# Kernel tuning notes

Measured on AMD Instinct MI355X. Metric: run time of the kernel, lower is better.

The kernel has to match this reference:

```python
import jax, jax.numpy as jnp
import numpy as np

H = 8  # head_count


def setup_inputs() -> dict:
    key = jax.random.key(0)
    ks = jax.random.split(key, 9)
    n, C, w = 8, 512, 8192
    Kc, Vc = 512, 512
    s = 0.02
    return {
        "x": jax.random.normal(ks[0], (n, C, w), dtype=jnp.float32),
        "Wk": jax.random.normal(ks[1], (Kc, C), dtype=jnp.float32) * s,
        "bk": jax.random.normal(ks[2], (Kc,), dtype=jnp.float32) * s,
        "Wq": jax.random.normal(ks[3], (Kc, C), dtype=jnp.float32) * s,
        "bq": jax.random.normal(ks[4], (Kc,), dtype=jnp.float32) * s,
        "Wv": jax.random.normal(ks[5], (Vc, C), dtype=jnp.float32) * s,
        "bv": jax.random.normal(ks[6], (Vc,), dtype=jnp.float32) * s,
        "Wr": jax.random.normal(ks[7], (C, Vc), dtype=jnp.float32) * s,
        "br": jax.random.normal(ks[8], (C,), dtype=jnp.float32) * s,
    }


def reference(x, Wk, bk, Wq, bq, Wv, bv, Wr, br):
    n, C, w = x.shape
    Kc, Vc = Wk.shape[0], Wv.shape[0]
    hk, hv = Kc // H, Vc // H
    # 1x1 Conv1d == channel-mixing GEMM
    keys = jnp.einsum('kc,ncw->nkw', Wk, x) + bk[None, :, None]
    queries = jnp.einsum('kc,ncw->nkw', Wq, x) + bq[None, :, None]
    values = jnp.einsum('vc,ncw->nvw', Wv, x) + bv[None, :, None]
    # split heads: [n, H, hd, w]
    K = jax.nn.softmax(keys.reshape(n, H, hk, w), axis=-1)   # softmax over positions
    Q = jax.nn.softmax(queries.reshape(n, H, hk, w), axis=2)  # softmax over channels
    V = values.reshape(n, H, hv, w)
    # context = K @ V^T : [n, H, hk, hv]
    ctx = jnp.einsum('nhkw,nhvw->nhkv', K, V)
    # attended = ctx^T @ Q : [n, H, hv, w]
    att = jnp.einsum('nhkv,nhkw->nhvw', ctx, Q).reshape(n, Vc, w)
    out = jnp.einsum('cv,nvw->ncw', Wr, att) + br[None, :, None] + x
    return out
```

## Files before the change

kernel.cpp:

```cpp
#include <hip/hip_runtime.h>
#include <hip/hip_bf16.h>
#include <cstdint>

#define NB 8
#define CD 512
#define WD 8192
#define NH 8

typedef __bf16 bf16x8 __attribute__((ext_vector_type(8)));
typedef float  f32x4  __attribute__((ext_vector_type(4)));
typedef float  f32x16 __attribute__((ext_vector_type(16)));

__device__ __forceinline__ void gload_lds16(const __bf16* g, __bf16* l) {
  __builtin_amdgcn_global_load_lds((const __attribute__((address_space(1))) void*)g,
                                   (__attribute__((address_space(3))) void*)l,
                                   16, 0, 0);
}

__global__ void __launch_bounds__(256) prep_x_kernel(const float* __restrict__ x,
                                                     __bf16* __restrict__ xT) {
  __shared__ float tile[64][65];
  const int n = blockIdx.z, cb = blockIdx.y * 64, wb = blockIdx.x * 64;
  const int t = threadIdx.x;
  const int t63 = t & 63, tg = t >> 6;
  const float* xp = x + ((size_t)n * CD + cb) * WD + wb;
#pragma unroll
  for (int i = 0; i < 16; i++) {
    const int cc = tg * 16 + i;
    tile[cc][t63] = xp[(size_t)cc * WD + t63];
  }
  __syncthreads();
  __bf16* op = xT + ((size_t)n * WD + wb) * CD + cb;
#pragma unroll
  for (int i = 0; i < 16; i++) {
    const int ww = tg * 16 + i;
    op[(size_t)ww * CD + t63] = (__bf16)tile[t63][ww];
  }
}

__global__ void __launch_bounds__(256) prep_w_kernel(const float* __restrict__ Wk,
                                                     const float* __restrict__ Wq,
                                                     const float* __restrict__ Wv,
                                                     const float* __restrict__ Wr,
                                                     const float* __restrict__ bk,
                                                     const float* __restrict__ bv,
                                                     __bf16* __restrict__ WkvB,
                                                     __bf16* __restrict__ WqB,
                                                     __bf16* __restrict__ WrB,
                                                     float* __restrict__ bkv) {
  const int gid = blockIdx.x * 256 + threadIdx.x;
  WkvB[gid]          = (__bf16)Wk[gid];
  WkvB[262144 + gid] = (__bf16)Wv[gid];
  WqB[gid]           = (__bf16)Wq[gid];
  WrB[gid]           = (__bf16)Wr[gid];
  if (gid < 512)       bkv[gid] = bk[gid];
  else if (gid < 1024) bkv[gid] = bv[gid - 512];
}

#define STAGE_SLAB(Ak, Bk, lds, t)                                          \
  _Pragma("unroll") for (int rnd = 0; rnd < 8; rnd++) {                     \
    const int c = rnd * 256 + (t);                                          \
    const int cc = c & 1023;                                                \
    const int r = cc >> 3;                                                  \
    const int g = (cc & 7) ^ (r & 7);                                       \
    const __bf16* src = ((c >> 10) ? (Bk) : (Ak)) + (size_t)r * 512 + g * 8;\
    gload_lds16(src, (lds) + (size_t)c * 8);                                \
  }

__device__ __forceinline__ void gemm_lds_core(const __bf16* __restrict__ A,
                                              const __bf16* __restrict__ B,
                                              f32x4 (&acc)[4][4], __bf16* lds) {
  const int t = threadIdx.x;
  const int lane = t & 63, wave = t >> 6;
  const int l15 = lane & 15, quad = lane >> 4;
  const int wm = (wave >> 1) << 6, wn = (wave & 1) << 6;
#pragma unroll 1
  for (int kc = 0; kc < 8; kc++) {
    const __bf16* Ak = A + kc * 64;
    const __bf16* Bk = B + kc * 64;
    STAGE_SLAB(Ak, Bk, lds, t)
    __syncthreads();
#pragma unroll
    for (int k0 = 0; k0 < 2; k0++) {
      const int gk = k0 * 4 + quad;
      bf16x8 av[4], bv[4];
#pragma unroll
      for (int i = 0; i < 4; i++) {
        const int r = wm + i * 16 + l15;
        av[i] = *(const bf16x8*)(lds + (size_t)((r << 3) + (gk ^ (r & 7))) * 8);
      }
#pragma unroll
      for (int j = 0; j < 4; j++) {
        const int r = wn + j * 16 + l15;
        bv[j] = *(const bf16x8*)(lds + (size_t)(8192 + (r << 3) + (gk ^ (r & 7))) * 8);
      }
#pragma unroll
      for (int i = 0; i < 4; i++)
#pragma unroll
        for (int j = 0; j < 4; j++)
          acc[i][j] = __builtin_amdgcn_mfma_f32_16x16x32_bf16(av[i], bv[j], acc[i][j], 0, 0, 0);
    }
    __syncthreads();
  }
}

__device__ __forceinline__ void gemm_lds_core32(const __bf16* __restrict__ A,
                                                const __bf16* __restrict__ B,
                                                f32x16 (&acc)[2][2], __bf16* lds) {
  const int t = threadIdx.x;
  const int lane = t & 63, wave = t >> 6;
  const int l31 = lane & 31, khalf = lane >> 5;
  const int wm = (wave >> 1) << 6, wn = (wave & 1) << 6;
#pragma unroll 1
  for (int kc = 0; kc < 8; kc++) {
    const __bf16* Ak = A + kc * 64;
    const __bf16* Bk = B + kc * 64;
    STAGE_SLAB(Ak, Bk, lds, t)
    __syncthreads();
#pragma unroll
    for (int kk = 0; kk < 4; kk++) {
      const int g = kk * 2 + khalf;
      bf16x8 av[2], bv[2];
#pragma unroll
      for (int i = 0; i < 2; i++) {
        const int r = wm + i * 32 + l31;
        av[i] = *(const bf16x8*)(lds + (size_t)((r << 3) + (g ^ (r & 7))) * 8);
      }
#pragma unroll
      for (int j = 0; j < 2; j++) {
        const int r = wn + j * 32 + l31;
        bv[j] = *(const bf16x8*)(lds + (size_t)(8192 + (r << 3) + (g ^ (r & 7))) * 8);
      }
#pragma unroll
      for (int i = 0; i < 2; i++)
#pragma unroll
        for (int j = 0; j < 2; j++)
          acc[i][j] = __builtin_amdgcn_mfma_f32_32x32x16_bf16(av[i], bv[j], acc[i][j], 0, 0, 0);
    }
    __syncthreads();
  }
}

__global__ void __launch_bounds__(256) gemm_kv_kernel(const __bf16* __restrict__ WkvB,
                                                      const __bf16* __restrict__ xT,
                                                      const float* __restrict__ bkv,
                                                      __bf16* __restrict__ kv) {
  __shared__ __bf16 lds[16384];
  const int n = blockIdx.z, m0 = blockIdx.y * 128, w0 = blockIdx.x * 128;
  f32x16 acc[2][2];
#pragma unroll
  for (int i = 0; i < 2; i++)
#pragma unroll
    for (int j = 0; j < 2; j++)
#pragma unroll
      for (int r = 0; r < 16; r++) acc[i][j][r] = 0.f;
  gemm_lds_core32(WkvB + (size_t)m0 * 512, xT + ((size_t)n * WD + w0) * 512, acc, lds);
  const int t = threadIdx.x, lane = t & 63, wave = t >> 6;
  const int l31 = lane & 31, khalf = lane >> 5;
  const int wm = (wave >> 1) << 6, wn = (wave & 1) << 6;
  __bf16* outp = kv + (size_t)n * 1024 * WD + w0 + wn + l31;
#pragma unroll
  for (int i = 0; i < 2; i++)
#pragma unroll
    for (int reg = 0; reg < 16; reg++) {
      const int row = (reg & 3) + 8 * (reg >> 2) + 4 * khalf;
      const int m = m0 + wm + i * 32 + row;
      const float bias = bkv[m];
      __bf16* rp = outp + (size_t)m * WD;
#pragma unroll
      for (int j = 0; j < 2; j++) rp[j * 32] = (__bf16)(acc[i][j][reg] + bias);
    }
}

__global__ void __launch_bounds__(256) gemm_qT_kernel(const __bf16* __restrict__ xT,
                                                      const __bf16* __restrict__ WqB,
                                                      const float* __restrict__ bq,
                                                      __bf16* __restrict__ qT) {
  __shared__ __bf16 lds[16384];
  const int n = blockIdx.z, w0 = blockIdx.x * 128, q0 = blockIdx.y * 128;
  f32x4 acc[4][4];
#pragma unroll
  for (int i = 0; i < 4; i++)
#pragma unroll
    for (int j = 0; j < 4; j++) acc[i][j] = (f32x4){0.f, 0.f, 0.f, 0.f};
  gemm_lds_core(xT + ((size_t)n * WD + w0) * 512, WqB + (size_t)q0 * 512, acc, lds);
  const int t = threadIdx.x, lane = t & 63, wave = t >> 6;
  const int l15 = lane & 15, quad = lane >> 4;
  const int wm = (wave >> 1) << 6, wn = (wave & 1) << 6;
  float bqv[4];
#pragma unroll
  for (int j = 0; j < 4; j++) bqv[j] = bq[q0 + wn + j * 16 + l15];
#pragma unroll
  for (int i = 0; i < 4; i++)
#pragma unroll
    for (int r = 0; r < 4; r++) {
      float e[4];
      float s = 0.f;
#pragma unroll
      for (int j = 0; j < 4; j++) {
        e[j] = __expf(acc[i][j][r] + bqv[j]);
        s += e[j];
      }
      s += __shfl_xor(s, 1);
      s += __shfl_xor(s, 2);
      s += __shfl_xor(s, 4);
      s += __shfl_xor(s, 8);
      const float inv = 1.0f / s;
      const int w = w0 + wm + i * 16 + quad * 4 + r;
      __bf16* rp = qT + ((size_t)n * WD + w) * 512 + q0 + wn + l15;
#pragma unroll
      for (int j = 0; j < 4; j++) rp[j * 16] = (__bf16)(e[j] * inv);
    }
}

__global__ void __launch_bounds__(256) gemm_out_kernel(const __bf16* __restrict__ Mf,
                                                       const __bf16* __restrict__ qT,
                                                       const float* __restrict__ br,
                                                       const float* __restrict__ x,
                                                       float* __restrict__ out) {
  __shared__ __bf16 lds[16384];
  const int n = blockIdx.z, c0 = blockIdx.y * 128, w0 = blockIdx.x * 128;
  f32x16 acc[2][2];
#pragma unroll
  for (int i = 0; i < 2; i++)
#pragma unroll
    for (int j = 0; j < 2; j++)
#pragma unroll
      for (int r = 0; r < 16; r++) acc[i][j][r] = 0.f;
  gemm_lds_core32(Mf + ((size_t)n * 512 + c0) * 512, qT + ((size_t)n * WD + w0) * 512, acc, lds);
  const int t = threadIdx.x, lane = t & 63, wave = t >> 6;
  const int l31 = lane & 31, khalf = lane >> 5;
  const int wm = (wave >> 1) << 6, wn = (wave & 1) << 6;
#pragma unroll
  for (int i = 0; i < 2; i++)
#pragma unroll
    for (int reg = 0; reg < 16; reg++) {
      const int row = (reg & 3) + 8 * (reg >> 2) + 4 * khalf;
      const int c = c0 + wm + i * 32 + row;
      const float bias = br[c];
      const size_t base = ((size_t)n * CD + c) * WD + w0 + wn + l31;
#pragma unroll
      for (int j = 0; j < 2; j++)
        out[base + j * 32] = acc[i][j][reg] + bias + x[base + j * 32];
    }
}

__global__ void __launch_bounds__(256) ctx_kernel(const __bf16* __restrict__ kv,
                                                  float* __restrict__ partial,
                                                  float* __restrict__ ssum) {
  const int chunk = blockIdx.x, h = blockIdx.y, n = blockIdx.z;
  const int t = threadIdx.x, lane = t & 63, wave = t >> 6;
  const int l15 = lane & 15, quad = lane >> 4;
  const int krow = h * 64 + wave * 16 + l15;
  const __bf16* Kp = kv + ((size_t)n * 1024 + krow) * WD + chunk * 1024 + quad * 8;
  const __bf16* Vp = kv + ((size_t)n * 1024 + 512 + h * 64 + l15) * WD + chunk * 1024 + quad * 8;
  f32x4 acc[4];
#pragma unroll
  for (int j = 0; j < 4; j++) acc[j] = (f32x4){0.f, 0.f, 0.f, 0.f};
  float esum = 0.f;
  for (int s = 0; s < 32; s++) {
    bf16x8 kraw = *(const bf16x8*)(Kp + s * 32);
    bf16x8 af;
#pragma unroll
    for (int e = 0; e < 8; e++) {
      const float ev = __expf((float)kraw[e]);
      esum += ev;
      af[e] = (__bf16)ev;
    }
#pragma unroll
    for (int j = 0; j < 4; j++) {
      bf16x8 bv = *(const bf16x8*)(Vp + (size_t)(j * 16) * WD + s * 32);
      acc[j] = __builtin_amdgcn_mfma_f32_16x16x32_bf16(af, bv, acc[j], 0, 0, 0);
    }
  }
  esum += __shfl_xor(esum, 16);
  esum += __shfl_xor(esum, 32);
  float* pp = partial + (((size_t)(n * 8 + h) * 8 + chunk) << 12);
#pragma unroll
  for (int j = 0; j < 4; j++)
#pragma unroll
    for (int r = 0; r < 4; r++) {
      const int kr = wave * 16 + quad * 4 + r;
      const int vc = j * 16 + l15;
      pp[kr * 64 + vc] = acc[j][r];
    }
  if (lane < 16)
    ssum[(((size_t)(n * 8 + h) * 8 + chunk) << 6) + wave * 16 + l15] = esum;
}

__global__ void __launch_bounds__(256) ctx_reduce_kernel(const float* __restrict__ partial,
                                                         const float* __restrict__ ssum,
                                                         __bf16* __restrict__ ctxB) {
  const int gid = blockIdx.x * 256 + threadIdx.x;
  const int nh = gid >> 12;
  const int kvi = gid & 4095;
  const int k = kvi >> 6;
  float s = 0.f;
#pragma unroll
  for (int c = 0; c < 8; c++) s += ssum[(((size_t)nh * 8 + c) << 6) + k];
  const float* pp = partial + ((size_t)nh << 15) + kvi;
  float v = 0.f;
#pragma unroll
  for (int c = 0; c < 8; c++) v += pp[(size_t)c << 12];
  ctxB[gid] = (__bf16)(v / s);
}

__global__ void __launch_bounds__(256) mfuse_kernel(const __bf16* __restrict__ WrB,
                                                    const __bf16* __restrict__ ctxB,
                                                    __bf16* __restrict__ Mf) {
  const int ms = blockIdx.x, h = blockIdx.y, n = blockIdx.z;
  const int t = threadIdx.x, lane = t & 63, wave = t >> 6;
  const int l15 = lane & 15, quad = lane >> 4;
  f32x4 acc[2][4];
#pragma unroll
  for (int i = 0; i < 2; i++)
#pragma unroll
    for (int j = 0; j < 4; j++) acc[i][j] = (f32x4){0.f, 0.f, 0.f, 0.f};
  const __bf16* Ap = WrB + (size_t)(ms * 128 + wave * 32 + l15) * 512 + h * 64 + quad * 8;
  const __bf16* Bp = ctxB + ((size_t)(n * 8 + h) << 12) + (size_t)l15 * 64 + quad * 8;
#pragma unroll
  for (int k0 = 0; k0 < 64; k0 += 32) {
    bf16x8 av[2];
#pragma unroll
    for (int i = 0; i < 2; i++) av[i] = *(const bf16x8*)(Ap + i * 16 * 512 + k0);
#pragma unroll
    for (int j = 0; j < 4; j++) {
      bf16x8 bv = *(const bf16x8*)(Bp + j * 16 * 64 + k0);
#pragma unroll
      for (int i = 0; i < 2; i++)
        acc[i][j] = __builtin_amdgcn_mfma_f32_16x16x32_bf16(av[i], bv, acc[i][j], 0, 0, 0);
    }
  }
#pragma unroll
  for (int i = 0; i < 2; i++)
#pragma unroll
    for (int j = 0; j < 4; j++)
#pragma unroll
      for (int r = 0; r < 4; r++) {
        const int c = ms * 128 + wave * 32 + i * 16 + quad * 4 + r;
        const int col = h * 64 + j * 16 + l15;
        Mf[((size_t)n * 512 + c) * 512 + col] = (__bf16)acc[i][j][r];
      }
}

extern "C" void kernel_launch(void* const* d_in, const int* in_sizes, int n_in,
                              void* d_out, int out_size, void* d_ws, size_t ws_size,
                              hipStream_t stream) {
  (void)in_sizes; (void)n_in; (void)out_size; (void)ws_size;
  const float* x  = (const float*)d_in[0];
  const float* Wk = (const float*)d_in[1];
  const float* bk = (const float*)d_in[2];
  const float* Wq = (const float*)d_in[3];
  const float* bq = (const float*)d_in[4];
  const float* Wv = (const float*)d_in[5];
  const float* bv = (const float*)d_in[6];
  const float* Wr = (const float*)d_in[7];
  const float* br = (const float*)d_in[8];
  float* out = (float*)d_out;

  char* ws = (char*)d_ws;
  __bf16* xT      = (__bf16*)ws;
  float*  partial = (float*)ws;
  __bf16* ctxB    = (__bf16*)(ws + (16ull << 20));
  __bf16* Mf      = (__bf16*)(ws + (20ull << 20));
  __bf16* kv      = (__bf16*)(ws + (64ull << 20));
  __bf16* qT      = (__bf16*)(ws + (192ull << 20));

  char* scr = (char*)d_out + (124ull << 20);
  __bf16* WkvB = (__bf16*)scr;
  __bf16* WqB  = (__bf16*)(scr + (1ull << 20));
  __bf16* WrB  = (__bf16*)(scr + (1536ull << 10));
  float*  bkv  = (float*)(scr + (2ull << 20));
  float*  ssum = (float*)(scr + (2ull << 20) + 65536);

  prep_x_kernel<<<dim3(128, 8, 8), 256, 0, stream>>>(x, xT);
  prep_w_kernel<<<dim3(1024), 256, 0, stream>>>(Wk, Wq, Wv, Wr, bk, bv, WkvB, WqB, WrB, bkv);
  gemm_kv_kernel<<<dim3(64, 8, 8), 256, 0, stream>>>(WkvB, xT, bkv, kv);
  gemm_qT_kernel<<<dim3(64, 4, 8), 256, 0, stream>>>(xT, WqB, bq, qT);
  ctx_kernel<<<dim3(8, 8, 8), 256, 0, stream>>>(kv, partial, ssum);
  ctx_reduce_kernel<<<dim3(1024), 256, 0, stream>>>(partial, ssum, ctxB);
  mfuse_kernel<<<dim3(4, 8, 8), 256, 0, stream>>>(WrB, ctxB, Mf);
  gemm_out_kernel<<<dim3(64, 4, 8), 256, 0, stream>>>(Mf, qT, br, x, out);
}
```

Before: 502.9 us.

## Rewrite KV projection GEMM with 256x256 tiles and double-buffered async LDS pipeline

Measured after the change: 515.3 us. 2.5% more time.

```diff
diff --git a/kernel.cpp b/kernel.cpp
--- a/kernel.cpp
+++ b/kernel.cpp
@@ -141,34 +141,138 @@
   }
 }
 
-__global__ void __launch_bounds__(256) gemm_kv_kernel(const __bf16* __restrict__ WkvB,
-                                                      const __bf16* __restrict__ xT,
-                                                      const float* __restrict__ bkv,
-                                                      __bf16* __restrict__ kv) {
-  __shared__ __bf16 lds[16384];
-  const int n = blockIdx.z, m0 = blockIdx.y * 128, w0 = blockIdx.x * 128;
-  f32x16 acc[2][2];
-#pragma unroll
-  for (int i = 0; i < 2; i++)
-#pragma unroll
-    for (int j = 0; j < 2; j++)
-#pragma unroll
-      for (int r = 0; r < 16; r++) acc[i][j][r] = 0.f;
-  gemm_lds_core32(WkvB + (size_t)m0 * 512, xT + ((size_t)n * WD + w0) * 512, acc, lds);
-  const int t = threadIdx.x, lane = t & 63, wave = t >> 6;
-  const int l31 = lane & 31, khalf = lane >> 5;
-  const int wm = (wave >> 1) << 6, wn = (wave & 1) << 6;
-  __bf16* outp = kv + (size_t)n * 1024 * WD + w0 + wn + l31;
-#pragma unroll
-  for (int i = 0; i < 2; i++)
-#pragma unroll
-    for (int reg = 0; reg < 16; reg++) {
-      const int row = (reg & 3) + 8 * (reg >> 2) + 4 * khalf;
-      const int m = m0 + wm + i * 32 + row;
+__device__ __forceinline__ void stage_chunk(const __bf16* __restrict__ g, __bf16* l, int row0) {
+  const int lane = threadIdx.x & 63;
+  const int r = row0 + (lane >> 3);
+  const int sg = lane & 7;
+  const int gk = sg ^ (r & 7);
+  gload_lds16(g + (size_t)r * 512 + gk * 8, l + (((r << 3) + sg) << 3));
+}
+
+__device__ __forceinline__ void stage_a_unit(const __bf16* __restrict__ g, __bf16* l, int u) {
+  const int w8 = (threadIdx.x >> 6) << 3;
+  stage_chunk(g, l, u * 64 + w8);
+  stage_chunk(g, l, 128 + u * 64 + w8);
+}
+
+__device__ __forceinline__ void stage_b_unit(const __bf16* __restrict__ g, __bf16* l, int v) {
+  const int w = threadIdx.x >> 6;
+  const int r0 = ((w & 3) << 3) + ((w >> 2) << 6) + (v << 5);
+  stage_chunk(g, l, r0);
+  stage_chunk(g, l, 128 + r0);
+}
+
+#define CKPT(N) asm volatile("s_waitcnt vmcnt(" #N ")" ::: "memory")
+
+#define PHASE(BSEL, MH, NH, STAGE_STMT, CKPT_STMT)                              \
+  do {                                                                          \
+    const __bf16* lA = lds + (BSEL) * 32768;                                    \
+    const __bf16* lB = lds + (BSEL) * 32768 + 16384;                            \
+    bf16x8 av[4][2], bv[2][2];                                                  \
+    _Pragma("unroll") for (int ks = 0; ks < 2; ks++) {                          \
+      const int gko = (ks * 4 + quad) ^ (l15 & 7);       \
+      _Pragma("unroll") for (int mi = 0; mi < 4; mi++) {                        \
+        const int r = wm128 + (MH) * 64 + mi * 16 + l15;                        \
+        av[mi][ks] = *(const bf16x8*)(lA + (((r << 3) + gko) << 3));            \
+      }                                                                         \
+      _Pragma("unroll") for (int nj = 0; nj < 2; nj++) {                        \
+        const int r = wn64 + (NH) * 32 + nj * 16 + l15;                         \
+        bv[nj][ks] = *(const bf16x8*)(lB + (((r << 3) + gko) << 3));            \
+      }                                                                         \
+    }                                                                           \
+    STAGE_STMT;                                                                 \
+    __builtin_amdgcn_s_barrier();                                               \
+    asm volatile("s_waitcnt lgkmcnt(0)" ::: "memory");                          \
+    __builtin_amdgcn_sched_barrier(0);                                          \
+    __builtin_amdgcn_s_setprio(1);                                              \
+    _Pragma("unroll") for (int ks = 0; ks < 2; ks++)                            \
+      _Pragma("unroll") for (int mi = 0; mi < 4; mi++)                          \
+        _Pragma("unroll") for (int nj = 0; nj < 2; nj++)                        \
+          acc[(MH) * 4 + mi][(NH) * 2 + nj] =                                   \
+              __builtin_amdgcn_mfma_f32_16x16x32_bf16(                          \
+                  av[mi][ks], bv[nj][ks], acc[(MH) * 4 + mi][(NH) * 2 + nj],    \
+                  0, 0, 0);                                                     \
+    __builtin_amdgcn_s_setprio(0);                                              \
+    CKPT_STMT;                                                                  \
+    __builtin_amdgcn_s_barrier();                                               \
+  } while (0)
+
+__global__ void __launch_bounds__(512, 2) gemm_kv_kernel(const __bf16* __restrict__ WkvB,
+                                                         const __bf16* __restrict__ xT,
+                                                         const float* __restrict__ bkv,
+                                                         __bf16* __restrict__ kv) {
+  extern __shared__ __bf16 lds[];
+  const int t = threadIdx.x;
+  const int lane = t & 63;
+  const int l15 = lane & 15, quad = lane >> 4;
+  const int wave = t >> 6;
+  const int wm128 = (wave >> 2) << 7;
+  const int wn64 = (wave & 3) << 6;
+
+  const int bid = blockIdx.x;
+  const int swz = (bid & 7) * 128 + (bid >> 3);
+  const int m0 = (swz & 3) << 8;
+  const int w0 = ((swz >> 2) & 31) << 8;
+  const int n = swz >> 7;
+
+  const __bf16* Ab = WkvB + (size_t)m0 * 512;
+  const __bf16* Bb = xT + ((size_t)n * WD + w0) * 512;
+
+  f32x4 acc[8][4];
+#pragma unroll
+  for (int i = 0; i < 8; i++)
+#pragma unroll
+    for (int j = 0; j < 4; j++) acc[i][j] = (f32x4){0.f, 0.f, 0.f, 0.f};
+
+  __bf16* const lA0 = lds;
+  __bf16* const lB0 = lds + 16384;
+  __bf16* const lA1 = lds + 32768;
+  __bf16* const lB1 = lds + 49152;
+
+  stage_a_unit(Ab, lA0, 0);
+  stage_b_unit(Bb, lB0, 0);
+  stage_a_unit(Ab, lA0, 1);
+  stage_b_unit(Bb, lB0, 1);
+  stage_a_unit(Ab + 64, lA1, 0);
+  stage_b_unit(Bb + 64, lB1, 0);
+  asm volatile("s_waitcnt vmcnt(4)" ::: "memory");
+  __builtin_amdgcn_s_barrier();
+
+#pragma unroll 1
+  for (int i = 0; i < 3; i++) {
+    const __bf16* As1 = Ab + (2 * i + 1) * 64;
+    const __bf16* Bs1 = Bb + (2 * i + 1) * 64;
+    const __bf16* As2 = Ab + (2 * i + 2) * 64;
+    const __bf16* Bs2 = Bb + (2 * i + 2) * 64;
+    const __bf16* As3 = Ab + (2 * i + 3) * 64;
+    const __bf16* Bs3 = Bb + (2 * i + 3) * 64;
+    PHASE(0, 0, 0, stage_a_unit(As1, lA1, 1), (void)0);
+    PHASE(0, 0, 1, stage_b_unit(Bs1, lB1, 1), (void)0);
+    PHASE(0, 1, 0, stage_a_unit(As2, lA0, 0), (void)0);
+    PHASE(0, 1, 1, stage_b_unit(Bs2, lB0, 0), CKPT(4));
+    PHASE(1, 0, 0, stage_a_unit(As2, lA0, 1), (void)0);
+    PHASE(1, 0, 1, stage_b_unit(Bs2, lB0, 1), (void)0);
+    PHASE(1, 1, 0, stage_a_unit(As3, lA1, 0), (void)0);
+    PHASE(1, 1, 1, stage_b_unit(Bs3, lB1, 0), CKPT(4));
+  }
+  PHASE(0, 0, 0, stage_a_unit(Ab + 7 * 64, lA1, 1), (void)0);
+  PHASE(0, 0, 1, stage_b_unit(Bb + 7 * 64, lB1, 1), (void)0);
+  PHASE(0, 1, 0, (void)0, (void)0);
+  PHASE(0, 1, 1, (void)0, CKPT(0));
+  PHASE(1, 0, 0, (void)0, (void)0);
+  PHASE(1, 0, 1, (void)0, (void)0);
+  PHASE(1, 1, 0, (void)0, (void)0);
+  PHASE(1, 1, 1, (void)0, (void)0);
+
+#pragma unroll
+  for (int MI = 0; MI < 8; MI++)
+#pragma unroll
+    for (int r = 0; r < 4; r++) {
+      const int m = m0 + wm128 + MI * 16 + quad * 4 + r;
       const float bias = bkv[m];
-      __bf16* rp = outp + (size_t)m * WD;
-#pragma unroll
-      for (int j = 0; j < 2; j++) rp[j * 32] = (__bf16)(acc[i][j][reg] + bias);
+      __bf16* rp = kv + ((size_t)n * 1024 + m) * WD + w0 + wn64 + l15;
+#pragma unroll
+      for (int j = 0; j < 4; j++) rp[j * 16] = (__bf16)(acc[MI][j][r] + bias);
     }
 }
 
@@ -375,7 +479,9 @@
 
   prep_x_kernel<<<dim3(128, 8, 8), 256, 0, stream>>>(x, xT);
   prep_w_kernel<<<dim3(1024), 256, 0, stream>>>(Wk, Wq, Wv, Wr, bk, bv, WkvB, WqB, WrB, bkv);
-  gemm_kv_kernel<<<dim3(64, 8, 8), 256, 0, stream>>>(WkvB, xT, bkv, kv);
+  hipFuncSetAttribute((const void*)gemm_kv_kernel,
+                      hipFuncAttributeMaxDynamicSharedMemorySize, 131072);
+  gemm_kv_kernel<<<dim3(1024), dim3(512), 131072, stream>>>(WkvB, xT, bkv, kv);
   gemm_qT_kernel<<<dim3(64, 4, 8), 256, 0, stream>>>(xT, WqB, bq, qT);
   ctx_kernel<<<dim3(8, 8, 8), 256, 0, stream>>>(kv, partial, ssum);
   ctx_reduce_kernel<<<dim3(1024), 256, 0, stream>>>(partial, ssum, ctxB);
```

## Merge KV and Q projection GEMMs, fuse ctx reduce with Mf, widen x transpose

Applied to the files above, without the earlier changes.

New measurement: 504.6 us. About the same (+0.3%).

```diff
diff --git a/kernel.cpp b/kernel.cpp
--- a/kernel.cpp
+++ b/kernel.cpp
@@ -7,6 +7,7 @@
 #define WD 8192
 #define NH 8
 
+typedef __bf16 bf16x2 __attribute__((ext_vector_type(2)));
 typedef __bf16 bf16x8 __attribute__((ext_vector_type(8)));
 typedef float  f32x4  __attribute__((ext_vector_type(4)));
 typedef float  f32x16 __attribute__((ext_vector_type(16)));
@@ -19,14 +20,14 @@
 
 __global__ void __launch_bounds__(256) prep_x_kernel(const float* __restrict__ x,
                                                      __bf16* __restrict__ xT) {
-  __shared__ float tile[64][65];
-  const int n = blockIdx.z, cb = blockIdx.y * 64, wb = blockIdx.x * 64;
+  __shared__ float tile[128][65];
+  const int n = blockIdx.z, cb = blockIdx.y * 128, wb = blockIdx.x * 64;
   const int t = threadIdx.x;
   const int t63 = t & 63, tg = t >> 6;
   const float* xp = x + ((size_t)n * CD + cb) * WD + wb;
 #pragma unroll
-  for (int i = 0; i < 16; i++) {
-    const int cc = tg * 16 + i;
+  for (int i = 0; i < 32; i++) {
+    const int cc = tg * 32 + i;
     tile[cc][t63] = xp[(size_t)cc * WD + t63];
   }
   __syncthreads();
@@ -34,7 +35,9 @@
 #pragma unroll
   for (int i = 0; i < 16; i++) {
     const int ww = tg * 16 + i;
-    op[(size_t)ww * CD + t63] = (__bf16)tile[t63][ww];
+    const float a = tile[t63 * 2][ww];
+    const float b = tile[t63 * 2 + 1][ww];
+    *(bf16x2*)(op + (size_t)ww * CD + t63 * 2) = (bf16x2){(__bf16)a, (__bf16)b};
   }
 }
 
@@ -141,76 +144,76 @@
   }
 }
 
-__global__ void __launch_bounds__(256) gemm_kv_kernel(const __bf16* __restrict__ WkvB,
-                                                      const __bf16* __restrict__ xT,
-                                                      const float* __restrict__ bkv,
-                                                      __bf16* __restrict__ kv) {
+__global__ void __launch_bounds__(256) gemm_kvq_kernel(const __bf16* __restrict__ WkvB,
+                                                       const __bf16* __restrict__ WqB,
+                                                       const __bf16* __restrict__ xT,
+                                                       const float* __restrict__ bkv,
+                                                       const float* __restrict__ bq,
+                                                       __bf16* __restrict__ kv,
+                                                       __bf16* __restrict__ qT) {
   __shared__ __bf16 lds[16384];
-  const int n = blockIdx.z, m0 = blockIdx.y * 128, w0 = blockIdx.x * 128;
-  f32x16 acc[2][2];
-#pragma unroll
-  for (int i = 0; i < 2; i++)
-#pragma unroll
-    for (int j = 0; j < 2; j++)
-#pragma unroll
-      for (int r = 0; r < 16; r++) acc[i][j][r] = 0.f;
-  gemm_lds_core32(WkvB + (size_t)m0 * 512, xT + ((size_t)n * WD + w0) * 512, acc, lds);
+  const int n = blockIdx.z, w0 = blockIdx.x * 128;
   const int t = threadIdx.x, lane = t & 63, wave = t >> 6;
-  const int l31 = lane & 31, khalf = lane >> 5;
-  const int wm = (wave >> 1) << 6, wn = (wave & 1) << 6;
-  __bf16* outp = kv + (size_t)n * 1024 * WD + w0 + wn + l31;
-#pragma unroll
-  for (int i = 0; i < 2; i++)
-#pragma unroll
-    for (int reg = 0; reg < 16; reg++) {
-      const int row = (reg & 3) + 8 * (reg >> 2) + 4 * khalf;
-      const int m = m0 + wm + i * 32 + row;
-      const float bias = bkv[m];
-      __bf16* rp = outp + (size_t)m * WD;
-#pragma unroll
-      for (int j = 0; j < 2; j++) rp[j * 32] = (__bf16)(acc[i][j][reg] + bias);
-    }
-}
-
-__global__ void __launch_bounds__(256) gemm_qT_kernel(const __bf16* __restrict__ xT,
-                                                      const __bf16* __restrict__ WqB,
-                                                      const float* __restrict__ bq,
-                                                      __bf16* __restrict__ qT) {
-  __shared__ __bf16 lds[16384];
-  const int n = blockIdx.z, w0 = blockIdx.x * 128, q0 = blockIdx.y * 128;
-  f32x4 acc[4][4];
-#pragma unroll
-  for (int i = 0; i < 4; i++)
-#pragma unroll
-    for (int j = 0; j < 4; j++) acc[i][j] = (f32x4){0.f, 0.f, 0.f, 0.f};
-  gemm_lds_core(xT + ((size_t)n * WD + w0) * 512, WqB + (size_t)q0 * 512, acc, lds);
-  const int t = threadIdx.x, lane = t & 63, wave = t >> 6;
-  const int l15 = lane & 15, quad = lane >> 4;
-  const int wm = (wave >> 1) << 6, wn = (wave & 1) << 6;
-  float bqv[4];
-#pragma unroll
-  for (int j = 0; j < 4; j++) bqv[j] = bq[q0 + wn + j * 16 + l15];
-#pragma unroll
-  for (int i = 0; i < 4; i++)
-#pragma unroll
-    for (int r = 0; r < 4; r++) {
-      float e[4];
-      float s = 0.f;
-#pragma unroll
-      for (int j = 0; j < 4; j++) {
-        e[j] = __expf(acc[i][j][r] + bqv[j]);
-        s += e[j];
-      }
-      s += __shfl_xor(s, 1);
-      s += __shfl_xor(s, 2);
-      s += __shfl_xor(s, 4);
-      s += __shfl_xor(s, 8);
-      const float inv = 1.0f / s;
-      const int w = w0 + wm + i * 16 + quad * 4 + r;
-      __bf16* rp = qT + ((size_t)n * WD + w) * 512 + q0 + wn + l15;
-#pragma unroll
-      for (int j = 0; j < 4; j++) rp[j * 16] = (__bf16)(e[j] * inv);
-    }
+
+  if (blockIdx.y < 8) {
+    const int m0 = blockIdx.y * 128;
+    f32x16 acc[2][2];
+#pragma unroll
+    for (int i = 0; i < 2; i++)
+#pragma unroll
+      for (int j = 0; j < 2; j++)
+#pragma unroll
+        for (int r = 0; r < 16; r++) acc[i][j][r] = 0.f;
+    gemm_lds_core32(WkvB + (size_t)m0 * 512, xT + ((size_t)n * WD + w0) * 512, acc, lds);
+    const int l31 = lane & 31, khalf = lane >> 5;
+    const int wm = (wave >> 1) << 6, wn = (wave & 1) << 6;
+    __bf16* outp = kv + (size_t)n * 1024 * WD + w0 + wn + l31;
+#pragma unroll
+    for (int i = 0; i < 2; i++)
+#pragma unroll
+      for (int reg = 0; reg < 16; reg++) {
+        const int row = (reg & 3) + 8 * (reg >> 2) + 4 * khalf;
+        const int m = m0 + wm + i * 32 + row;
+        const float bias = bkv[m];
+        __bf16* rp = outp + (size_t)m * WD;
+#pragma unroll
+        for (int j = 0; j < 2; j++) rp[j * 32] = (__bf16)(acc[i][j][reg] + bias);
+      }
+  } else {
+    const int q0 = (blockIdx.y - 8) * 128;
+    f32x4 acc[4][4];
+#pragma unroll
+    for (int i = 0; i < 4; i++)
+#pragma unroll
+      for (int j = 0; j < 4; j++) acc[i][j] = (f32x4){0.f, 0.f, 0.f, 0.f};
+    gemm_lds_core(xT + ((size_t)n * WD + w0) * 512, WqB + (size_t)q0 * 512, acc, lds);
+    const int l15 = lane & 15, quad = lane >> 4;
+    const int wm = (wave >> 1) << 6, wn = (wave & 1) << 6;
+    float bqv[4];
+#pragma unroll
+    for (int j = 0; j < 4; j++) bqv[j] = bq[q0 + wn + j * 16 + l15];
+#pragma unroll
+    for (int i = 0; i < 4; i++)
+#pragma unroll
+      for (int r = 0; r < 4; r++) {
+        float e[4];
+        float s = 0.f;
+#pragma unroll
+        for (int j = 0; j < 4; j++) {
+          e[j] = __expf(acc[i][j][r] + bqv[j]);
+          s += e[j];
+        }
+        s += __shfl_xor(s, 1);
+        s += __shfl_xor(s, 2);
+        s += __shfl_xor(s, 4);
+        s += __shfl_xor(s, 8);
+        const float inv = 1.0f / s;
+        const int w = w0 + wm + i * 16 + quad * 4 + r;
+        __bf16* rp = qT + ((size_t)n * WD + w) * 512 + q0 + wn + l15;
+#pragma unroll
+        for (int j = 0; j < 4; j++) rp[j * 16] = (__bf16)(e[j] * inv);
+      }
+  }
 }
 
 __global__ void __launch_bounds__(256) gemm_out_kernel(const __bf16* __restrict__ Mf,
@@ -288,59 +291,66 @@
     ssum[(((size_t)(n * 8 + h) * 8 + chunk) << 6) + wave * 16 + l15] = esum;
 }
 
-__global__ void __launch_bounds__(256) ctx_reduce_kernel(const float* __restrict__ partial,
+__global__ void __launch_bounds__(256) ctx_finish_kernel(const float* __restrict__ partial,
                                                          const float* __restrict__ ssum,
-                                                         __bf16* __restrict__ ctxB) {
-  const int gid = blockIdx.x * 256 + threadIdx.x;
-  const int nh = gid >> 12;
-  const int kvi = gid & 4095;
-  const int k = kvi >> 6;
-  float s = 0.f;
-#pragma unroll
-  for (int c = 0; c < 8; c++) s += ssum[(((size_t)nh * 8 + c) << 6) + k];
-  const float* pp = partial + ((size_t)nh << 15) + kvi;
-  float v = 0.f;
-#pragma unroll
-  for (int c = 0; c < 8; c++) v += pp[(size_t)c << 12];
-  ctxB[gid] = (__bf16)(v / s);
-}
-
-__global__ void __launch_bounds__(256) mfuse_kernel(const __bf16* __restrict__ WrB,
-                                                    const __bf16* __restrict__ ctxB,
-                                                    __bf16* __restrict__ Mf) {
-  const int ms = blockIdx.x, h = blockIdx.y, n = blockIdx.z;
-  const int t = threadIdx.x, lane = t & 63, wave = t >> 6;
+                                                         const __bf16* __restrict__ WrB,
+                                                         __bf16* __restrict__ Mf) {
+  __shared__ __bf16 ctx_tile[64][72];
+  __shared__ float srow[64];
+  const int h = blockIdx.x, n = blockIdx.y;
+  const int nh = n * 8 + h;
+  const int t = threadIdx.x;
+  if (t < 64) {
+    float s = 0.f;
+#pragma unroll
+    for (int c = 0; c < 8; c++) s += ssum[(((size_t)nh * 8 + c) << 6) + t];
+    srow[t] = 1.0f / s;
+  }
+  __syncthreads();
+  const float* pp = partial + ((size_t)nh << 15);
+#pragma unroll
+  for (int i = 0; i < 16; i++) {
+    const int kvi = i * 256 + t;
+    float v = 0.f;
+#pragma unroll
+    for (int c = 0; c < 8; c++) v += pp[((size_t)c << 12) + kvi];
+    ctx_tile[kvi >> 6][kvi & 63] = (__bf16)(v * srow[kvi >> 6]);
+  }
+  __syncthreads();
+  const int lane = t & 63, wave = t >> 6;
   const int l15 = lane & 15, quad = lane >> 4;
-  f32x4 acc[2][4];
-#pragma unroll
-  for (int i = 0; i < 2; i++)
-#pragma unroll
-    for (int j = 0; j < 4; j++) acc[i][j] = (f32x4){0.f, 0.f, 0.f, 0.f};
-  const __bf16* Ap = WrB + (size_t)(ms * 128 + wave * 32 + l15) * 512 + h * 64 + quad * 8;
-  const __bf16* Bp = ctxB + ((size_t)(n * 8 + h) << 12) + (size_t)l15 * 64 + quad * 8;
-#pragma unroll
-  for (int k0 = 0; k0 < 64; k0 += 32) {
-    bf16x8 av[2];
-#pragma unroll
-    for (int i = 0; i < 2; i++) av[i] = *(const bf16x8*)(Ap + i * 16 * 512 + k0);
-#pragma unroll
-    for (int j = 0; j < 4; j++) {
-      bf16x8 bv = *(const bf16x8*)(Bp + j * 16 * 64 + k0);
-#pragma unroll
-      for (int i = 0; i < 2; i++)
-        acc[i][j] = __builtin_amdgcn_mfma_f32_16x16x32_bf16(av[i], bv, acc[i][j], 0, 0, 0);
-    }
-  }
-#pragma unroll
-  for (int i = 0; i < 2; i++)
-#pragma unroll
-    for (int j = 0; j < 4; j++)
-#pragma unroll
-      for (int r = 0; r < 4; r++) {
-        const int c = ms * 128 + wave * 32 + i * 16 + quad * 4 + r;
-        const int col = h * 64 + j * 16 + l15;
-        Mf[((size_t)n * 512 + c) * 512 + col] = (__bf16)acc[i][j][r];
-      }
+#pragma unroll 1
+  for (int ms = 0; ms < 4; ms++) {
+    f32x4 acc[2][4];
+#pragma unroll
+    for (int i = 0; i < 2; i++)
+#pragma unroll
+      for (int j = 0; j < 4; j++) acc[i][j] = (f32x4){0.f, 0.f, 0.f, 0.f};
+    const __bf16* Ap = WrB + (size_t)(ms * 128 + wave * 32 + l15) * 512 + h * 64 + quad * 8;
+#pragma unroll
+    for (int k0 = 0; k0 < 64; k0 += 32) {
+      bf16x8 av[2];
+#pragma unroll
+      for (int i = 0; i < 2; i++) av[i] = *(const bf16x8*)(Ap + i * 16 * 512 + k0);
+#pragma unroll
+      for (int j = 0; j < 4; j++) {
+        bf16x8 bv = *(const bf16x8*)(&ctx_tile[j * 16 + l15][quad * 8 + k0]);
+#pragma unroll
+        for (int i = 0; i < 2; i++)
+          acc[i][j] = __builtin_amdgcn_mfma_f32_16x16x32_bf16(av[i], bv, acc[i][j], 0, 0, 0);
+      }
+    }
+#pragma unroll
+    for (int i = 0; i < 2; i++)
+#pragma unroll
+      for (int j = 0; j < 4; j++)
+#pragma unroll
+        for (int r = 0; r < 4; r++) {
+          const int c = ms * 128 + wave * 32 + i * 16 + quad * 4 + r;
+          const int col = h * 64 + j * 16 + l15;
+          Mf[((size_t)n * 512 + c) * 512 + col] = (__bf16)acc[i][j][r];
+        }
+  }
 }
 
 extern "C" void kernel_launch(void* const* d_in, const int* in_sizes, int n_in,
@@ -361,7 +371,6 @@
   char* ws = (char*)d_ws;
   __bf16* xT      = (__bf16*)ws;
   float*  partial = (float*)ws;
-  __bf16* ctxB    = (__bf16*)(ws + (16ull << 20));
   __bf16* Mf      = (__bf16*)(ws + (20ull << 20));
   __bf16* kv      = (__bf16*)(ws + (64ull << 20));
   __bf16* qT      = (__bf16*)(ws + (192ull << 20));
@@ -373,12 +382,10 @@
   float*  bkv  = (float*)(scr + (2ull << 20));
   float*  ssum = (float*)(scr + (2ull << 20) + 65536);
 
-  prep_x_kernel<<<dim3(128, 8, 8), 256, 0, stream>>>(x, xT);
+  prep_x_kernel<<<dim3(128, 4, 8), 256, 0, stream>>>(x, xT);
   prep_w_kernel<<<dim3(1024), 256, 0, stream>>>(Wk, Wq, Wv, Wr, bk, bv, WkvB, WqB, WrB, bkv);
-  gemm_kv_kernel<<<dim3(64, 8, 8), 256, 0, stream>>>(WkvB, xT, bkv, kv);
-  gemm_qT_kernel<<<dim3(64, 4, 8), 256, 0, stream>>>(xT, WqB, bq, qT);
+  gemm_kvq_kernel<<<dim3(64, 12, 8), 256, 0, stream>>>(WkvB, WqB, xT, bkv, bq, kv, qT);
   ctx_kernel<<<dim3(8, 8, 8), 256, 0, stream>>>(kv, partial, ssum);
-  ctx_reduce_kernel<<<dim3(1024), 256, 0, stream>>>(partial, ssum, ctxB);
-  mfuse_kernel<<<dim3(4, 8, 8), 256, 0, stream>>>(WrB, ctxB, Mf);
+  ctx_finish_kernel<<<dim3(8, 8), 256, 0, stream>>>(partial, ssum, WrB, Mf);
   gemm_out_kernel<<<dim3(64, 4, 8), 256, 0, stream>>>(Mf, qT, br, x, out);
 }
```
